# Performance work log

Measured on AMD Instinct MI355X. Metric: run time of the kernel, lower is better.

The kernel has to match this reference:

```python
import jax, jax.numpy as jnp
import numpy as np

INV_SQRT2 = np.float32(2.0 ** -0.5)
EPS = 1e-5


def _bn5(x, g, b, m, v):
    # inference-mode BatchNorm3d over channel axis 1 of NCDHW
    r = (1, -1, 1, 1, 1)
    return (x - m.reshape(r)) * (g.reshape(r) * jax.lax.rsqrt(v.reshape(r) + EPS)) + b.reshape(r)


def _conv3d(x, w, b, dil=1, pad=0):
    out = jax.lax.conv_general_dilated(
        x, w, window_strides=(1, 1, 1), padding=[(pad, pad)] * 3,
        rhs_dilation=(dil, dil, dil),
        dimension_numbers=('NCDHW', 'OIDHW', 'NCDHW'))
    return out + b.reshape(1, -1, 1, 1, 1)


def _haar_dwt2(x):
    # pywt dwt2(x, 'haar', axes=(-3,-2)) for even-length axes.
    # axis -3 (D): a = approx, d = detail (pywt sign: (x0 - x1)/sqrt2)
    a = (x[:, :, 0::2] + x[:, :, 1::2]) * INV_SQRT2
    d = (x[:, :, 0::2] - x[:, :, 1::2]) * INV_SQRT2
    # axis -2 (H)
    LL = (a[:, :, :, 0::2] + a[:, :, :, 1::2]) * INV_SQRT2  # 'aa'
    HL = (a[:, :, :, 0::2] - a[:, :, :, 1::2]) * INV_SQRT2  # 'ad'
    LH = (d[:, :, :, 0::2] + d[:, :, :, 1::2]) * INV_SQRT2  # 'da'
    HH = (d[:, :, :, 0::2] - d[:, :, :, 1::2]) * INV_SQRT2  # 'dd'
    return LL, LH, HL, HH


def setup_inputs() -> dict:
    key = jax.random.key(0)
    ks = jax.random.split(key, 12)
    B, C1, D, H, W = 2, 60, 128, 128, 64
    CH, R = 64, 4  # gate channels, CH // reduction_ratio
    f32 = jnp.float32
    inp = {
        'x1': jax.random.normal(ks[0], (B, C1, D // 2, H // 2, W), f32),
        'x2': jax.random.normal(ks[1], (B, 1, D, H, W), f32),
        # BatchNorm3d(4) on dwt features
        'bn_g': jnp.ones(4, f32), 'bn_b': jnp.zeros(4, f32),
        'bn_m': jnp.zeros(4, f32), 'bn_v': jnp.ones(4, f32),
        # BAM channel gate: Linear(64->4), BN1d(4), Linear(4->64)
        'cg_w1': jax.random.normal(ks[2], (R, CH), f32) * 0.05,
        'cg_b1': jnp.zeros(R, f32),
        'cg_bng': jnp.ones(R, f32), 'cg_bnb': jnp.zeros(R, f32),
        'cg_bnm': jnp.zeros(R, f32), 'cg_bnv': jnp.ones(R, f32),
        'cg_w2': jax.random.normal(ks[3], (CH, R), f32) * 0.05,
        'cg_b2': jnp.zeros(CH, f32),
        # BAM spatial gate
        'sg_w0': jax.random.normal(ks[4], (R, CH, 1, 1, 1), f32) * 0.05,
        'sg_b0': jnp.zeros(R, f32),
        'sg_g0': jnp.ones(R, f32), 'sg_be0': jnp.zeros(R, f32),
        'sg_m0': jnp.zeros(R, f32), 'sg_v0': jnp.ones(R, f32),
        'sg_w1': jax.random.normal(ks[5], (R, R, 3, 3, 3), f32) * 0.05,
        'sg_b1': jnp.zeros(R, f32),
        'sg_g1': jnp.ones(R, f32), 'sg_be1': jnp.zeros(R, f32),
        'sg_m1': jnp.zeros(R, f32), 'sg_v1': jnp.ones(R, f32),
        'sg_w2': jax.random.normal(ks[6], (R, R, 3, 3, 3), f32) * 0.05,
        'sg_b2': jnp.zeros(R, f32),
        'sg_g2': jnp.ones(R, f32), 'sg_be2': jnp.zeros(R, f32),
        'sg_m2': jnp.zeros(R, f32), 'sg_v2': jnp.ones(R, f32),
        'sg_w3': jax.random.normal(ks[7], (1, R, 1, 1, 1), f32) * 0.05,
        'sg_b3': jnp.zeros(1, f32),
    }
    return inp


def reference(x1, x2, bn_g, bn_b, bn_m, bn_v,
              cg_w1, cg_b1, cg_bng, cg_bnb, cg_bnm, cg_bnv, cg_w2, cg_b2,
              sg_w0, sg_b0, sg_g0, sg_be0, sg_m0, sg_v0,
              sg_w1, sg_b1, sg_g1, sg_be1, sg_m1, sg_v1,
              sg_w2, sg_b2, sg_g2, sg_be2, sg_m2, sg_v2,
              sg_w3, sg_b3):
    LL, LH, HL, HH = _haar_dwt2(x2)
    dwt = jnp.concatenate([LL, LH, HL, HH], axis=1)          # [B,4,D/2,H/2,W]
    dwt = jax.nn.relu(_bn5(dwt, bn_g, bn_b, bn_m, bn_v))
    feat = jnp.concatenate([dwt, x1], axis=1)                # [B,64,D/2,H/2,W]

    # BAM channel gate
    pooled = feat.mean(axis=(2, 3, 4))                        # [B,64]
    h = pooled @ cg_w1.T + cg_b1
    h = jax.nn.relu((h - cg_bnm) * (cg_bng * jax.lax.rsqrt(cg_bnv + EPS)) + cg_bnb)
    att_c = (h @ cg_w2.T + cg_b2)[:, :, None, None, None]     # [B,64,1,1,1]

    # BAM spatial gate
    s = jax.nn.relu(_bn5(_conv3d(feat, sg_w0, sg_b0), sg_g0, sg_be0, sg_m0, sg_v0))
    s = jax.nn.relu(_bn5(_conv3d(s, sg_w1, sg_b1, dil=4, pad=4), sg_g1, sg_be1, sg_m1, sg_v1))
    s = jax.nn.relu(_bn5(_conv3d(s, sg_w2, sg_b2, dil=4, pad=4), sg_g2, sg_be2, sg_m2, sg_v2))
    att_s = _conv3d(s, sg_w3, sg_b3)                          # [B,1,D/2,H/2,W]

    scale = 1.0 + jax.nn.sigmoid(att_c + att_s)
    return (feat * scale, LL)
```

## Files before the change

### kernel.cpp

```cpp
#include <hip/hip_runtime.h>
#include <math.h>

#define EPSBN 1e-5f

typedef float f32x2 __attribute__((ext_vector_type(2)));
typedef float f32x4 __attribute__((ext_vector_type(4)));

constexpr int B   = 2;
constexpr int C1  = 60;
constexpr int NV  = 64 * 64 * 64;
constexpr int NBa = NV / 512;

__global__ __launch_bounds__(256) void kA(
    const float* __restrict__ x1, const float* __restrict__ x2,
    const float* __restrict__ bn_g, const float* __restrict__ bn_b,
    const float* __restrict__ bn_m, const float* __restrict__ bn_v,
    const float* __restrict__ sg_w0, const float* __restrict__ sg_b0,
    const float* __restrict__ sg_g0, const float* __restrict__ sg_be0,
    const float* __restrict__ sg_m0, const float* __restrict__ sg_v0,
    float* __restrict__ dwtM, float* __restrict__ s0,
    float* __restrict__ part, float* __restrict__ outLL)
{
    __shared__ float wsumq[64][65];

    const int tid = threadIdx.x;
    const int qid = tid >> 2;

    float dsc[4], dsh[4], c0A[4], c0B[4];
    #pragma unroll
    for (int r = 0; r < 4; ++r) {
        float d = bn_g[r] * rsqrtf(bn_v[r] + EPSBN);
        dsc[r] = d; dsh[r] = bn_b[r] - bn_m[r] * d;
        float sc = sg_g0[r] * rsqrtf(sg_v0[r] + EPSBN);
        c0A[r] = sc; c0B[r] = (sg_b0[r] - sg_m0[r]) * sc + sg_be0[r];
    }

    const int b = blockIdx.y;
    const int v = blockIdx.x * 512 + tid * 2;
    const int x = v & 63, y = (v >> 6) & 63, z = v >> 12;

    const float* px2 = x2 + (size_t)b * (128 * 128 * 64);
    const size_t i00 = ((size_t)(2 * z) * 128 + 2 * y) * 64 + x;
    const float2 p00 = *(const float2*)(px2 + i00);
    const float2 p01 = *(const float2*)(px2 + i00 + 64);
    const float2 p10 = *(const float2*)(px2 + i00 + 8192);
    const float2 p11 = *(const float2*)(px2 + i00 + 8256);
    const float* q00 = (const float*)&p00; const float* q01 = (const float*)&p01;
    const float* q10 = (const float*)&p10; const float* q11 = (const float*)&p11;

    float tv[2][4], llv[2];
    #pragma unroll
    for (int vi = 0; vi < 2; ++vi) {
        float a = q00[vi], bb = q01[vi], c = q10[vi], d = q11[vi];
        float LL = 0.5f * (a + bb + c + d);
        float LH = 0.5f * (a + bb - c - d);
        float HL = 0.5f * (a - bb + c - d);
        float HH = 0.5f * (a - bb - c + d);
        llv[vi] = LL;
        tv[vi][0] = fmaxf(LL * dsc[0] + dsh[0], 0.f);
        tv[vi][1] = fmaxf(LH * dsc[1] + dsh[1], 0.f);
        tv[vi][2] = fmaxf(HL * dsc[2] + dsh[2], 0.f);
        tv[vi][3] = fmaxf(HH * dsc[3] + dsh[3], 0.f);
    }
    {
        f32x2 ll2 = { llv[0], llv[1] };
        __builtin_nontemporal_store(ll2, (f32x2*)(outLL + (size_t)b * NV + v));
    }

    float acc[2][4] = {};
    #pragma unroll
    for (int c = 0; c < 4; ++c) {
        #pragma unroll
        for (int vi = 0; vi < 2; ++vi) {
            float t = tv[vi][c];
            #pragma unroll
            for (int r = 0; r < 4; ++r) acc[vi][r] += sg_w0[r * 64 + c] * t;
        }
        float rs = tv[0][c] + tv[1][c];
        rs += __shfl_xor(rs, 1);
        rs += __shfl_xor(rs, 2);
        if ((tid & 3) == 0) wsumq[c][qid] = rs;
        *(float2*)(dwtM + ((size_t)b * 4 + c) * NV + v) = make_float2(tv[0][c], tv[1][c]);
    }

    const float* px1 = x1 + (size_t)b * C1 * NV + v;
    #pragma unroll 2
    for (int c = 0; c < C1; ++c) {
        const float2 f = *(const float2*)(px1 + (size_t)c * NV);
        #pragma unroll
        for (int r = 0; r < 4; ++r) {
            const float w = sg_w0[r * 64 + 4 + c];
            acc[0][r] += w * f.x;
            acc[1][r] += w * f.y;
        }
        float rs = f.x + f.y;
        rs += __shfl_xor(rs, 1);
        rs += __shfl_xor(rs, 2);
        if ((tid & 3) == 0) wsumq[4 + c][qid] = rs;
    }

    float4* ps0 = (float4*)s0 + (size_t)b * NV + v;
    #pragma unroll
    for (int vi = 0; vi < 2; ++vi)
        ps0[vi] = make_float4(fmaxf(acc[vi][0] * c0A[0] + c0B[0], 0.f),
                              fmaxf(acc[vi][1] * c0A[1] + c0B[1], 0.f),
                              fmaxf(acc[vi][2] * c0A[2] + c0B[2], 0.f),
                              fmaxf(acc[vi][3] * c0A[3] + c0B[3], 0.f));

    __syncthreads();
    if (tid < 64) {
        const float* rowp = &wsumq[tid][0];
        float p = 0.f;
        #pragma unroll
        for (int i = 0; i < 64; ++i) p += rowp[i];
        part[((size_t)b * 64 + tid) * NBa + blockIdx.x] = p;
    }
}

__global__ __launch_bounds__(256) void kConv1(
    const float* __restrict__ sin_,
    const float* __restrict__ w, const float* __restrict__ bias,
    const float* __restrict__ g, const float* __restrict__ be,
    const float* __restrict__ m, const float* __restrict__ vv,
    const float* __restrict__ part,
    const float* __restrict__ cg_w1, const float* __restrict__ cg_b1,
    const float* __restrict__ cg_bng, const float* __restrict__ cg_bnb,
    const float* __restrict__ cg_bnm, const float* __restrict__ cg_bnv,
    const float* __restrict__ cg_w2, const float* __restrict__ cg_b2,
    float* __restrict__ ec,
    float* __restrict__ outp)
{
    const int tid = threadIdx.x;
    const int b = blockIdx.y;

    if (blockIdx.x == NBa) {
        __shared__ float pooled[64];
        __shared__ float h[4];
        const int c = tid >> 2, q = tid & 3;
        const float4* pp = (const float4*)(part + ((size_t)b * 64 + c) * NBa + q * 128);
        float sm = 0.f;
        #pragma unroll
        for (int i = 0; i < 32; ++i) { float4 f = pp[i]; sm += f.x + f.y + f.z + f.w; }
        sm += __shfl_xor(sm, 1);
        sm += __shfl_xor(sm, 2);
        if (q == 0) pooled[c] = sm * (1.0f / NV);
        __syncthreads();
        if (tid < 4) {
            float a = cg_b1[tid];
            for (int cc = 0; cc < 64; ++cc) a += pooled[cc] * cg_w1[tid * 64 + cc];
            float sc = cg_bng[tid] * rsqrtf(cg_bnv[tid] + EPSBN);
            h[tid] = fmaxf((a - cg_bnm[tid]) * sc + cg_bnb[tid], 0.f);
        }
        __syncthreads();
        if (tid < 64) {
            float a = cg_b2[tid];
            #pragma unroll
            for (int r = 0; r < 4; ++r) a += h[r] * cg_w2[tid * 4 + r];
            ec[b * 64 + tid] = __expf(-a);
        }
        return;
    }

    __shared__ float4 wl4[108];
    if (tid < 108) {
        const int t = tid >> 2, r = tid & 3;
        wl4[tid] = make_float4(w[r * 108 +      t], w[r * 108 +  27 + t],
                               w[r * 108 + 54 + t], w[r * 108 +  81 + t]);
    }
    float cAr[4], cBr[4];
    #pragma unroll
    for (int r = 0; r < 4; ++r) {
        float sc = g[r] * rsqrtf(vv[r] + EPSBN);
        cAr[r] = sc;
        cBr[r] = (bias[r] - m[r]) * sc + be[r];
    }
    __syncthreads();

    const int v = blockIdx.x * 512 + tid * 2;
    const int x = v & 63, y = (v >> 6) & 63, z = v >> 12;
    const float4* pin = (const float4*)sin_ + (size_t)b * NV;

    float acc[2][4] = {};
    #pragma unroll
    for (int kz = -1; kz <= 1; ++kz) {
        const int zz = z + 4 * kz;
        if ((unsigned)zz >= 64u) continue;
        #pragma unroll
        for (int ky = -1; ky <= 1; ++ky) {
            const int yy = y + 4 * ky;
            if ((unsigned)yy >= 64u) continue;
            #pragma unroll
            for (int kx = -1; kx <= 1; ++kx) {
                const int xx = x + 4 * kx;
                if ((unsigned)xx >= 64u) continue;
                const int t = (kz + 1) * 9 + (ky + 1) * 3 + (kx + 1);
                const int vt = zz * 4096 + yy * 64 + xx;
                const float4 w0 = wl4[t * 4 + 0];
                const float4 w1 = wl4[t * 4 + 1];
                const float4 w2 = wl4[t * 4 + 2];
                const float4 w3 = wl4[t * 4 + 3];
                #pragma unroll
                for (int vi = 0; vi < 2; ++vi) {
                    const float4 tap = pin[vt + vi];
                    acc[vi][0] += w0.x * tap.x + w0.y * tap.y + w0.z * tap.z + w0.w * tap.w;
                    acc[vi][1] += w1.x * tap.x + w1.y * tap.y + w1.z * tap.z + w1.w * tap.w;
                    acc[vi][2] += w2.x * tap.x + w2.y * tap.y + w2.z * tap.z + w2.w * tap.w;
                    acc[vi][3] += w3.x * tap.x + w3.y * tap.y + w3.z * tap.z + w3.w * tap.w;
                }
            }
        }
    }

    float4* po = (float4*)outp + (size_t)b * NV + v;
    #pragma unroll
    for (int vi = 0; vi < 2; ++vi)
        po[vi] = make_float4(fmaxf(acc[vi][0] * cAr[0] + cBr[0], 0.f),
                             fmaxf(acc[vi][1] * cAr[1] + cBr[1], 0.f),
                             fmaxf(acc[vi][2] * cAr[2] + cBr[2], 0.f),
                             fmaxf(acc[vi][3] * cAr[3] + cBr[3], 0.f));
}

__global__ __launch_bounds__(256) void kConv2(
    const float* __restrict__ sin_,
    const float* __restrict__ w, const float* __restrict__ bias,
    const float* __restrict__ g, const float* __restrict__ be,
    const float* __restrict__ m, const float* __restrict__ vv,
    const float* __restrict__ w3, const float* __restrict__ b3,
    float* __restrict__ es)
{
    const int tid = threadIdx.x;
    __shared__ float4 wl4[108];
    if (tid < 108) {
        const int t = tid >> 2, r = tid & 3;
        wl4[tid] = make_float4(w[r * 108 +      t], w[r * 108 +  27 + t],
                               w[r * 108 + 54 + t], w[r * 108 +  81 + t]);
    }
    float cAr[4], cBr[4], w3l[4];
    #pragma unroll
    for (int r = 0; r < 4; ++r) {
        float sc = g[r] * rsqrtf(vv[r] + EPSBN);
        cAr[r] = sc;
        cBr[r] = (bias[r] - m[r]) * sc + be[r];
        w3l[r] = w3[r];
    }
    const float b3l = b3[0];
    __syncthreads();

    const int b = blockIdx.y;
    const int v = blockIdx.x * 512 + tid * 2;
    const int x = v & 63, y = (v >> 6) & 63, z = v >> 12;
    const float4* pin = (const float4*)sin_ + (size_t)b * NV;

    float acc[2][4] = {};
    #pragma unroll
    for (int kz = -1; kz <= 1; ++kz) {
        const int zz = z + 4 * kz;
        if ((unsigned)zz >= 64u) continue;
        #pragma unroll
        for (int ky = -1; ky <= 1; ++ky) {
            const int yy = y + 4 * ky;
            if ((unsigned)yy >= 64u) continue;
            #pragma unroll
            for (int kx = -1; kx <= 1; ++kx) {
                const int xx = x + 4 * kx;
                if ((unsigned)xx >= 64u) continue;
                const int t = (kz + 1) * 9 + (ky + 1) * 3 + (kx + 1);
                const int vt = zz * 4096 + yy * 64 + xx;
                const float4 w0 = wl4[t * 4 + 0];
                const float4 w1 = wl4[t * 4 + 1];
                const float4 w2 = wl4[t * 4 + 2];
                const float4 w3q = wl4[t * 4 + 3];
                #pragma unroll
                for (int vi = 0; vi < 2; ++vi) {
                    const float4 tap = pin[vt + vi];
                    acc[vi][0] += w0.x * tap.x + w0.y * tap.y + w0.z * tap.z + w0.w * tap.w;
                    acc[vi][1] += w1.x * tap.x + w1.y * tap.y + w1.z * tap.z + w1.w * tap.w;
                    acc[vi][2] += w2.x * tap.x + w2.y * tap.y + w2.z * tap.z + w2.w * tap.w;
                    acc[vi][3] += w3q.x * tap.x + w3q.y * tap.y + w3q.z * tap.z + w3q.w * tap.w;
                }
            }
        }
    }

    float ev[2];
    #pragma unroll
    for (int vi = 0; vi < 2; ++vi) {
        float r0 = fmaxf(acc[vi][0] * cAr[0] + cBr[0], 0.f);
        float r1 = fmaxf(acc[vi][1] * cAr[1] + cBr[1], 0.f);
        float r2 = fmaxf(acc[vi][2] * cAr[2] + cBr[2], 0.f);
        float r3 = fmaxf(acc[vi][3] * cAr[3] + cBr[3], 0.f);
        ev[vi] = __expf(-(b3l + w3l[0] * r0 + w3l[1] * r1 + w3l[2] * r2 + w3l[3] * r3));
    }
    *(float2*)(es + (size_t)b * NV + v) = make_float2(ev[0], ev[1]);
}

__global__ __launch_bounds__(256) void kMul(
    const float* __restrict__ x1,
    const float* __restrict__ dwtM,
    const float* __restrict__ es,
    const float* __restrict__ ec,
    float* __restrict__ out0)
{
    const int i0 = blockIdx.x * 256 + threadIdx.x;
    #pragma unroll 4
    for (int it = 0; it < 16; ++it) {
        const size_t idx = (size_t)i0 + (size_t)it * 524288;
        const int b  = (int)(idx >> 22);
        const int r  = (int)(idx & 4194303);
        const int c  = r >> 16;
        const int vq = r & 65535;
        const float* base = (c < 4)
            ? dwtM + ((size_t)b * 4 + c) * NV
            : x1   + ((size_t)b * C1 + (c - 4)) * NV;
        const float4 in4 = *(const float4*)(base + (size_t)vq * 4);
        const float4 es4 = ((const float4*)(es + (size_t)b * NV))[vq];
        const float  e   = ec[(b << 6) + c];
        f32x4 o;
        o.x = in4.x * (1.f + __builtin_amdgcn_rcpf(1.f + e * es4.x));
        o.y = in4.y * (1.f + __builtin_amdgcn_rcpf(1.f + e * es4.y));
        o.z = in4.z * (1.f + __builtin_amdgcn_rcpf(1.f + e * es4.z));
        o.w = in4.w * (1.f + __builtin_amdgcn_rcpf(1.f + e * es4.w));
        __builtin_nontemporal_store(o, (f32x4*)out0 + idx);
    }
}

extern "C" void kernel_launch(void* const* d_in, const int* in_sizes, int n_in,
                              void* d_out, int out_size, void* d_ws, size_t ws_size,
                              hipStream_t stream)
{
    const float* x1 = (const float*)d_in[0];
    const float* x2 = (const float*)d_in[1];
    const float* bn_g = (const float*)d_in[2];
    const float* bn_b = (const float*)d_in[3];
    const float* bn_m = (const float*)d_in[4];
    const float* bn_v = (const float*)d_in[5];
    const float* cg_w1 = (const float*)d_in[6];
    const float* cg_b1 = (const float*)d_in[7];
    const float* cg_bng = (const float*)d_in[8];
    const float* cg_bnb = (const float*)d_in[9];
    const float* cg_bnm = (const float*)d_in[10];
    const float* cg_bnv = (const float*)d_in[11];
    const float* cg_w2 = (const float*)d_in[12];
    const float* cg_b2 = (const float*)d_in[13];
    const float* sg_w0 = (const float*)d_in[14];
    const float* sg_b0 = (const float*)d_in[15];
    const float* sg_g0 = (const float*)d_in[16];
    const float* sg_be0 = (const float*)d_in[17];
    const float* sg_m0 = (const float*)d_in[18];
    const float* sg_v0 = (const float*)d_in[19];
    const float* sg_w1 = (const float*)d_in[20];
    const float* sg_b1 = (const float*)d_in[21];
    const float* sg_g1 = (const float*)d_in[22];
    const float* sg_be1 = (const float*)d_in[23];
    const float* sg_m1 = (const float*)d_in[24];
    const float* sg_v1 = (const float*)d_in[25];
    const float* sg_w2 = (const float*)d_in[26];
    const float* sg_b2 = (const float*)d_in[27];
    const float* sg_g2 = (const float*)d_in[28];
    const float* sg_be2 = (const float*)d_in[29];
    const float* sg_m2 = (const float*)d_in[30];
    const float* sg_v2 = (const float*)d_in[31];
    const float* sg_w3 = (const float*)d_in[32];
    const float* sg_b3 = (const float*)d_in[33];

    float* ws = (float*)d_ws;
    float* dwtM = ws;
    float* s0   = ws + 2097152;
    float* s1   = ws + 4194304;
    float* es   = ws + 6291456;
    float* part = ws + 6815744;
    float* ec   = ws + 6881280;

    float* out0  = (float*)d_out;
    float* outLL = out0 + (size_t)B * 64 * NV;

    dim3 blk(256);
    kA<<<dim3(NBa, B), blk, 0, stream>>>(x1, x2, bn_g, bn_b, bn_m, bn_v,
                                         sg_w0, sg_b0, sg_g0, sg_be0, sg_m0, sg_v0,
                                         dwtM, s0, part, outLL);
    kConv1<<<dim3(NBa + 1, B), blk, 0, stream>>>(s0, sg_w1, sg_b1, sg_g1, sg_be1, sg_m1, sg_v1,
                                                 part, cg_w1, cg_b1, cg_bng, cg_bnb, cg_bnm, cg_bnv,
                                                 cg_w2, cg_b2, ec, s1);
    kConv2<<<dim3(NBa, B), blk, 0, stream>>>(s1, sg_w2, sg_b2, sg_g2, sg_be2, sg_m2, sg_v2,
                                             sg_w3, sg_b3, es);
    kMul<<<dim3(2048), blk, 0, stream>>>(x1, dwtM, es, ec, out0);
}
```

Measured before the change: 108.2 us.

## Fuse final dilated conv and sigmoid gate into the output multiply kernel

Merges the second dilated conv plus the 1x1 projection and exp into the output scaling kernel. Spatial attention is computed in registers instead of being written to and read back from workspace, and one kernel launch is removed. The channel-gate values are cached in shared memory. The two thread halves of each block recompute the same conv for different channel ranges, so the conv arithmetic and the s1 reads are doubled.

```diff
diff --git a/kernel.cpp b/kernel.cpp
--- a/kernel.cpp
+++ b/kernel.cpp
@@ -220,21 +220,29 @@
                              fmaxf(acc[vi][3] * cAr[3] + cBr[3], 0.f));
 }
 
-__global__ __launch_bounds__(256) void kConv2(
-    const float* __restrict__ sin_,
+__global__ __launch_bounds__(256) void kMulF(
+    const float* __restrict__ x1,
+    const float* __restrict__ dwtM,
+    const float* __restrict__ s1,
     const float* __restrict__ w, const float* __restrict__ bias,
     const float* __restrict__ g, const float* __restrict__ be,
     const float* __restrict__ m, const float* __restrict__ vv,
     const float* __restrict__ w3, const float* __restrict__ b3,
-    float* __restrict__ es)
+    const float* __restrict__ ec,
+    float* __restrict__ out0)
 {
     const int tid = threadIdx.x;
+    const int b = blockIdx.x >> 9;
+    const int blockBase = (blockIdx.x & 511) * 128;
+
     __shared__ float4 wl4[108];
+    __shared__ float ecs[64];
     if (tid < 108) {
         const int t = tid >> 2, r = tid & 3;
         wl4[tid] = make_float4(w[r * 108 +      t], w[r * 108 +  27 + t],
                                w[r * 108 + 54 + t], w[r * 108 +  81 + t]);
     }
+    if (tid < 64) ecs[tid] = ec[b * 64 + tid];
     float cAr[4], cBr[4], w3l[4];
     #pragma unroll
     for (int r = 0; r < 4; ++r) {
@@ -246,12 +254,13 @@
     const float b3l = b3[0];
     __syncthreads();
 
-    const int b = blockIdx.y;
-    const int v = blockIdx.x * 512 + tid * 2;
-    const int x = v & 63, y = (v >> 6) & 63, z = v >> 12;
-    const float4* pin = (const float4*)sin_ + (size_t)b * NV;
-
-    float acc[2][4] = {};
+    const int vq = blockBase + (tid & 127);
+    const int v  = vq * 4;
+    const int x0 = v & 63, y = (v >> 6) & 63, z = v >> 12;
+    const int ch0 = (tid >> 7) * 32;
+
+    const float4* pin = (const float4*)s1 + (size_t)b * NV;
+    float acc[4][4] = {};
     #pragma unroll
     for (int kz = -1; kz <= 1; ++kz) {
         const int zz = z + 4 * kz;
@@ -262,16 +271,16 @@
             if ((unsigned)yy >= 64u) continue;
             #pragma unroll
             for (int kx = -1; kx <= 1; ++kx) {
-                const int xx = x + 4 * kx;
-                if ((unsigned)xx >= 64u) continue;
+                const int xb = x0 + 4 * kx;
+                if ((unsigned)xb >= 64u) continue;
                 const int t = (kz + 1) * 9 + (ky + 1) * 3 + (kx + 1);
-                const int vt = zz * 4096 + yy * 64 + xx;
+                const int vt = zz * 4096 + yy * 64 + xb;
                 const float4 w0 = wl4[t * 4 + 0];
                 const float4 w1 = wl4[t * 4 + 1];
                 const float4 w2 = wl4[t * 4 + 2];
                 const float4 w3q = wl4[t * 4 + 3];
                 #pragma unroll
-                for (int vi = 0; vi < 2; ++vi) {
+                for (int vi = 0; vi < 4; ++vi) {
                     const float4 tap = pin[vt + vi];
                     acc[vi][0] += w0.x * tap.x + w0.y * tap.y + w0.z * tap.z + w0.w * tap.w;
                     acc[vi][1] += w1.x * tap.x + w1.y * tap.y + w1.z * tap.z + w1.w * tap.w;
@@ -282,45 +291,31 @@
         }
     }
 
-    float ev[2];
-    #pragma unroll
-    for (int vi = 0; vi < 2; ++vi) {
+    float es[4];
+    #pragma unroll
+    for (int vi = 0; vi < 4; ++vi) {
         float r0 = fmaxf(acc[vi][0] * cAr[0] + cBr[0], 0.f);
         float r1 = fmaxf(acc[vi][1] * cAr[1] + cBr[1], 0.f);
         float r2 = fmaxf(acc[vi][2] * cAr[2] + cBr[2], 0.f);
         float r3 = fmaxf(acc[vi][3] * cAr[3] + cBr[3], 0.f);
-        ev[vi] = __expf(-(b3l + w3l[0] * r0 + w3l[1] * r1 + w3l[2] * r2 + w3l[3] * r3));
-    }
-    *(float2*)(es + (size_t)b * NV + v) = make_float2(ev[0], ev[1]);
-}
-
-__global__ __launch_bounds__(256) void kMul(
-    const float* __restrict__ x1,
-    const float* __restrict__ dwtM,
-    const float* __restrict__ es,
-    const float* __restrict__ ec,
-    float* __restrict__ out0)
-{
-    const int i0 = blockIdx.x * 256 + threadIdx.x;
+        es[vi] = __expf(-(b3l + w3l[0] * r0 + w3l[1] * r1 + w3l[2] * r2 + w3l[3] * r3));
+    }
+
+    float* po = out0 + ((size_t)b * 64 + ch0) * NV + v;
     #pragma unroll 4
-    for (int it = 0; it < 16; ++it) {
-        const size_t idx = (size_t)i0 + (size_t)it * 524288;
-        const int b  = (int)(idx >> 22);
-        const int r  = (int)(idx & 4194303);
-        const int c  = r >> 16;
-        const int vq = r & 65535;
-        const float* base = (c < 4)
+    for (int cc = 0; cc < 32; ++cc) {
+        const int c = ch0 + cc;
+        const float* basep = (c < 4)
             ? dwtM + ((size_t)b * 4 + c) * NV
             : x1   + ((size_t)b * C1 + (c - 4)) * NV;
-        const float4 in4 = *(const float4*)(base + (size_t)vq * 4);
-        const float4 es4 = ((const float4*)(es + (size_t)b * NV))[vq];
-        const float  e   = ec[(b << 6) + c];
+        const float4 in4 = *(const float4*)(basep + v);
+        const float e = ecs[c];
         f32x4 o;
-        o.x = in4.x * (1.f + __builtin_amdgcn_rcpf(1.f + e * es4.x));
-        o.y = in4.y * (1.f + __builtin_amdgcn_rcpf(1.f + e * es4.y));
-        o.z = in4.z * (1.f + __builtin_amdgcn_rcpf(1.f + e * es4.z));
-        o.w = in4.w * (1.f + __builtin_amdgcn_rcpf(1.f + e * es4.w));
-        __builtin_nontemporal_store(o, (f32x4*)out0 + idx);
+        o.x = in4.x * (1.f + __builtin_amdgcn_rcpf(1.f + e * es[0]));
+        o.y = in4.y * (1.f + __builtin_amdgcn_rcpf(1.f + e * es[1]));
+        o.z = in4.z * (1.f + __builtin_amdgcn_rcpf(1.f + e * es[2]));
+        o.w = in4.w * (1.f + __builtin_amdgcn_rcpf(1.f + e * es[3]));
+        __builtin_nontemporal_store(o, (f32x4*)(po + (size_t)cc * NV));
     }
 }
 
@@ -367,9 +362,8 @@
     float* dwtM = ws;
     float* s0   = ws + 2097152;
     float* s1   = ws + 4194304;
-    float* es   = ws + 6291456;
-    float* part = ws + 6815744;
-    float* ec   = ws + 6881280;
+    float* part = ws + 6291456;
+    float* ec   = ws + 6356992;
 
     float* out0  = (float*)d_out;
     float* outLL = out0 + (size_t)B * 64 * NV;
@@ -381,7 +375,6 @@
     kConv1<<<dim3(NBa + 1, B), blk, 0, stream>>>(s0, sg_w1, sg_b1, sg_g1, sg_be1, sg_m1, sg_v1,
                                                  part, cg_w1, cg_b1, cg_bng, cg_bnb, cg_bnm, cg_bnv,
                                                  cg_w2, cg_b2, ec, s1);
-    kConv2<<<dim3(NBa, B), blk, 0, stream>>>(s1, sg_w2, sg_b2, sg_g2, sg_be2, sg_m2, sg_v2,
-                                             sg_w3, sg_b3, es);
-    kMul<<<dim3(2048), blk, 0, stream>>>(x1, dwtM, es, ec, out0);
+    kMulF<<<dim3(1024), blk, 0, stream>>>(x1, dwtM, s1, sg_w2, sg_b2, sg_g2, sg_be2, sg_m2, sg_v2,
+                                          sg_w3, sg_b3, ec, out0);
 }
```

Measured after the change: 112.3 us. +3.8%, slower.
